# Optimization experiments

Hardware: AMD Instinct MI355X
Metric: run time of the kernel (lower is better)

Reference implementation:

```python
import jax, jax.numpy as jnp
import numpy as np

EPS = 1e-08
PARTIAL_NORM = 1.5
TOPK = 8
SELF_MOD_STEPS = 2


def _layernorm(x, g, b, eps=1e-05):
    mu = jnp.mean(x, axis=-1, keepdims=True)
    var = jnp.mean((x - mu) ** 2, axis=-1, keepdims=True)
    return (x - mu) / jnp.sqrt(var + eps) * g + b


def _spectral_normalize(w, iters=10):
    # mimic torch spectral_norm: divide by top singular value (power iteration)
    u = jnp.ones((w.shape[0],), w.dtype) / np.sqrt(w.shape[0])
    def step(u, _):
        v = w.T @ u
        v = v / (jnp.linalg.norm(v) + 1e-12)
        u2 = w @ v
        u2 = u2 / (jnp.linalg.norm(u2) + 1e-12)
        return u2, None
    u, _ = jax.lax.scan(step, u, None, length=iters)
    v = w.T @ u
    v = v / (jnp.linalg.norm(v) + 1e-12)
    sigma = u @ (w @ v)
    return w / sigma


def setup_inputs() -> dict:
    B, D, H, S, C = 8192, 2048, 1024, 3, 1000
    P = 1024  # proj_dim = ((max(H, D//2)+7)//8)*8
    key = jax.random.key(0)
    ks = jax.random.split(key, 16)
    x = jax.random.normal(ks[0], (B, D), jnp.float32)
    proj_w = jax.random.normal(ks[1], (P, D), jnp.float32) / np.sqrt(D)
    proj_b = jnp.zeros((P,), jnp.float32)
    ln_p_g = jnp.ones((P,), jnp.float32)
    ln_p_b = jnp.zeros((P,), jnp.float32)
    wf_w = jax.random.normal(ks[2], (S, 2 * H, P), jnp.float32) / np.sqrt(P)
    wf_w = jax.vmap(_spectral_normalize)(wf_w)
    wf_b = jax.random.normal(ks[3], (S, 2 * H), jnp.float32) * 0.02
    ln_g = jnp.ones((S, 2 * H), jnp.float32)
    ln_b = jnp.zeros((S, 2 * H), jnp.float32)
    temperature = jnp.ones((1,), jnp.float32)
    phases = jax.random.normal(ks[4], (S, 1), jnp.float32) * 0.5
    gate_w = jax.random.normal(ks[5], (H, H), jnp.float32) / np.sqrt(H)
    gate_b = jnp.zeros((H,), jnp.float32)
    cls_w1 = jax.random.normal(ks[6], (H, H), jnp.float32) / np.sqrt(H)
    cls_b1 = jnp.zeros((H,), jnp.float32)
    cls_w2 = jax.random.normal(ks[7], (C, H), jnp.float32) / np.sqrt(H)
    cls_b2 = jnp.zeros((C,), jnp.float32).at[1].set(0.75)
    return {"x": x, "proj_w": proj_w, "proj_b": proj_b, "ln_p_g": ln_p_g,
            "ln_p_b": ln_p_b, "wf_w": wf_w, "wf_b": wf_b, "ln_g": ln_g,
            "ln_b": ln_b, "temperature": temperature, "phases": phases,
            "gate_w": gate_w, "gate_b": gate_b, "cls_w1": cls_w1,
            "cls_b1": cls_b1, "cls_w2": cls_w2, "cls_b2": cls_b2}


def reference(x, proj_w, proj_b, ln_p_g, ln_p_b, wf_w, wf_b, ln_g, ln_b,
              temperature, phases, gate_w, gate_b, cls_w1, cls_b1, cls_w2, cls_b2):
    H = wf_w.shape[1] // 2
    # input projection (dropout is identity at eval)
    h = jax.nn.gelu(_layernorm(x @ proj_w.T + proj_b, ln_p_g, ln_p_b), approximate=False)
    # all wavefunctions at once: [B, S, 2H]
    out = jnp.einsum('bp,sep->bse', h, wf_w) + wf_b[None]
    out = _layernorm(out, ln_g[None], ln_b[None])
    out = jnp.exp(-out * out)  # ArcBell
    alpha, beta = out[..., :H], out[..., H:]
    norm_sq = jnp.sum(alpha ** 2 + beta ** 2, axis=-1, keepdims=True) + EPS
    factor = jnp.sqrt(PARTIAL_NORM ** 2 / norm_sq)
    alpha = alpha * factor
    beta = beta * factor
    phase = phases[None]  # [1, S, 1]
    c, s = jnp.cos(phase), jnp.sin(phase)
    wave_r = alpha * c - beta * s  # [B, S, H]
    wave_i = alpha * s + beta * c
    # cosine-similarity interference weights
    mean_real = jnp.mean(wave_r, axis=1)  # [B, H]
    mean_norm = jnp.sqrt(jnp.sum(mean_real ** 2, axis=-1, keepdims=True)) + EPS  # [B,1]
    wave_norms = jnp.sqrt(jnp.sum(wave_r ** 2, axis=-1, keepdims=True)) + EPS  # [B,S,1]
    dot = jnp.sum(wave_r * mean_real[:, None], axis=-1, keepdims=True)  # [B,S,1]
    cos_sim = (dot / (wave_norms * mean_norm[:, None]))[..., 0]  # [B,S]
    w = jax.nn.softmax(cos_sim / temperature, axis=1)[..., None]  # [B,S,1]
    sup_r = jnp.sum(wave_r * w, axis=1)  # [B,H]
    sup_i = jnp.sum(wave_i * w, axis=1)
    # self-modulation with leaky residual
    for _ in range(SELF_MOD_STEPS):
        mag = jnp.sqrt(sup_r ** 2 + sup_i ** 2 + EPS)
        gate = jax.nn.sigmoid(mag @ gate_w.T + gate_b)
        sup_r = sup_r * gate + sup_r * 0.1
        sup_i = sup_i * gate + sup_i * 0.1
    mag_sq = sup_r ** 2 + sup_i ** 2
    # top-k mask + scatter + renormalize
    _, inds = jax.lax.top_k(mag_sq, TOPK)
    rows = jnp.arange(mag_sq.shape[0])[:, None]
    mask = jnp.zeros_like(mag_sq).at[rows, inds].set(1.0)
    masked = mag_sq * mask
    probs = masked / (jnp.sum(masked, axis=-1, keepdims=True) + EPS)
    # classifier (dropout identity at eval)
    hid = jax.nn.gelu(probs @ cls_w1.T + cls_b1, approximate=False)
    logits = hid @ cls_w2.T + cls_b2
    return logits
```

## Files before the change

kernel.cpp:

```cpp
#include <hip/hip_runtime.h>
#include <cstdint>

typedef __attribute__((ext_vector_type(8))) __bf16 bf16x8;
typedef __attribute__((ext_vector_type(4))) __bf16 bf16x4;
typedef __attribute__((ext_vector_type(4))) float f32x4;
typedef unsigned long long u64;

__device__ __forceinline__ void gld_lds16(const void* g, void* l) {
  __builtin_amdgcn_global_load_lds(
      (const __attribute__((address_space(1))) void*)g,
      (__attribute__((address_space(3))) void*)l, 16, 0, 0);
}

__device__ __forceinline__ float block_sum(float v, float* scr) {
#pragma unroll
  for (int off = 32; off > 0; off >>= 1) v += __shfl_down(v, off, 64);
  const int w = threadIdx.x >> 6;
  __syncthreads();
  if ((threadIdx.x & 63) == 0) scr[w] = v;
  __syncthreads();
  float s = 0.f;
  const int nw = blockDim.x >> 6;
  for (int i = 0; i < nw; ++i) s += scr[i];
  return s;
}

template <int N>
__device__ __forceinline__ void block_sumN(float* v, float* scr) {
#pragma unroll
  for (int i = 0; i < N; ++i)
#pragma unroll
    for (int m = 1; m < 64; m <<= 1) v[i] += __shfl_xor(v[i], m, 64);
  const int w = threadIdx.x >> 6;
  __syncthreads();
  if ((threadIdx.x & 63) == 0)
#pragma unroll
    for (int i = 0; i < N; ++i) scr[w * N + i] = v[i];
  __syncthreads();
#pragma unroll
  for (int i = 0; i < N; ++i) {
    float s = 0.f;
    for (int ww = 0; ww < 4; ++ww) s += scr[ww * N + i];
    v[i] = s;
  }
}

__device__ __forceinline__ float gelu_fast(float x) {
  const float ax = fabsf(x) * 0.70710678118654752f;
  const float t = 1.f / (1.f + 0.3275911f * ax);
  const float e = __expf(-ax * ax);
  float poly = 1.061405429f;
  poly = poly * t - 1.453152027f;
  poly = poly * t + 1.421413741f;
  poly = poly * t - 0.284496736f;
  poly = poly * t + 0.254829592f;
  const float erfax = 1.f - poly * t * e;
  const float er = copysignf(erfax, x);
  return 0.5f * x * (1.f + er);
}

__global__ __launch_bounds__(256) void k_cast_bf16(const float* __restrict__ in,
                                                   __bf16* __restrict__ out) {
  const long i = ((long)blockIdx.x * 256 + threadIdx.x) * 4;
  f32x4 v = *(const f32x4*)(in + i);
  bf16x4 o = {(__bf16)v[0], (__bf16)v[1], (__bf16)v[2], (__bf16)v[3]};
  *(bf16x4*)(out + i) = o;
}

__global__ __launch_bounds__(256) void k_cast_weights(
    const float* __restrict__ pw, __bf16* __restrict__ w1b,
    const float* __restrict__ wfw, __bf16* __restrict__ wfwb,
    const float* __restrict__ gw, __bf16* __restrict__ gwb) {
  const int bid = blockIdx.x;
  const float* in;
  __bf16* out;
  long base;
  if (bid < 2048) { in = pw; out = w1b; base = (long)bid * 1024; }
  else if (bid < 8192) { in = wfw; out = wfwb; base = (long)(bid - 2048) * 1024; }
  else { in = gw; out = gwb; base = (long)(bid - 8192) * 1024; }
  const long i = base + threadIdx.x * 4;
  f32x4 v = *(const f32x4*)(in + i);
  bf16x4 o = {(__bf16)v[0], (__bf16)v[1], (__bf16)v[2], (__bf16)v[3]};
  *(bf16x4*)(out + i) = o;
}

__global__ __launch_bounds__(256) void k_cast_pad(const float* __restrict__ in,
                                                  __bf16* __restrict__ out,
                                                  int rows_real, int cols) {
  const long i = ((long)blockIdx.x * 256 + threadIdx.x) * 4;
  const int row = (int)(i / cols);
  const int col = (int)(i % cols);
  bf16x4 o;
  if (row < rows_real) {
    f32x4 v = *(const f32x4*)(in + (long)row * cols + col);
    o = (bf16x4){(__bf16)v[0], (__bf16)v[1], (__bf16)v[2], (__bf16)v[3]};
  } else {
    o = (bf16x4){(__bf16)0.f, (__bf16)0.f, (__bf16)0.f, (__bf16)0.f};
  }
  *(bf16x4*)(out + i) = o;
}

__global__ __launch_bounds__(256) void k_transpose1k(const float* __restrict__ in,
                                                     float* __restrict__ out) {
  __shared__ float t[32][33];
  const int tx = threadIdx.x & 31;
  const int ty = threadIdx.x >> 5;
  const int r0 = blockIdx.y * 32, c0 = blockIdx.x * 32;
#pragma unroll
  for (int k = 0; k < 4; ++k)
    t[ty + 8 * k][tx] = in[(long)(r0 + ty + 8 * k) * 1024 + c0 + tx];
  __syncthreads();
#pragma unroll
  for (int k = 0; k < 4; ++k)
    out[(long)(c0 + ty + 8 * k) * 1024 + r0 + tx] = t[tx][ty + 8 * k];
}

__global__ __launch_bounds__(512, 1) void k_gemm256_bt(
    const __bf16* __restrict__ A, const __bf16* __restrict__ B,
    const float* __restrict__ bias, __bf16* __restrict__ C,
    int M, int N, int K) {
  __shared__ __align__(16) __bf16 lds[2][2][256 * 64];
  const int tid = threadIdx.x;
  const int lane = tid & 63;
  const int wid = tid >> 6;
  const int wr = wid >> 2;
  const int wc = wid & 3;
  const int gx = gridDim.x, gy = gridDim.y;
  const int lin = blockIdx.y * gx + blockIdx.x;
  const int xcd = lin & 7;
  const int local = lin >> 3;
  const int byq = gy >> 3;
  const int bx = local / byq;
  const int by = xcd * byq + (local % byq);
  const int m0 = by * 256, n0 = bx * 256;
  const int fr = lane & 15;
  const int fx = lane >> 4;
  const int px = lane & 7;

  const __bf16* Abase = A + (long)m0 * K;
  const __bf16* Bbase = B + (long)n0 * K;

  auto stage_q = [&](int slot, int kt, int mat, int half) {
    const __bf16* src = (mat ? Bbase : Abase) + kt * 64;
#pragma unroll
    for (int q = 0; q < 2; ++q) {
      const int idx = q * 512 + tid;
      const int r = idx >> 3;
      const int pblk = idx & 7;
      const int row = half * 128 + r;
      const int lblk = pblk ^ (r & 7);
      gld_lds16(src + (long)row * K + lblk * 8,
                (char*)&lds[slot][mat][row * 64 + pblk * 8]);
    }
  };
  auto frag = [&](int slot, int mat, int row, int ks) -> bf16x8 {
    return *(const bf16x8*)&lds[slot][mat][row * 64 + ((((ks << 2) + fx) ^ px) << 3)];
  };

  f32x4 acc[8][4] = {};
  const int nt = K >> 6;
#pragma unroll
  for (int qp = 0; qp < 4; ++qp) stage_q(0, 0, qp >> 1, qp & 1);

  const int arow = wr * 128 + fr;
  const int brow = wc * 64 + fr;

  for (int t = 0; t < nt; ++t) {
    const int sc = t & 1, sn = sc ^ 1;
    if (t + 1 < nt) {
#pragma unroll
      for (int qp = 0; qp < 4; ++qp) stage_q(sn, t + 1, qp >> 1, qp & 1);
      asm volatile("s_waitcnt vmcnt(8)" ::: "memory");
    } else {
      asm volatile("s_waitcnt vmcnt(0)" ::: "memory");
    }
    __builtin_amdgcn_sched_barrier(0);
    __builtin_amdgcn_s_barrier();
    bf16x8 b0[4], b1[4];
#pragma unroll
    for (int j = 0; j < 4; ++j) {
      b0[j] = frag(sc, 1, brow + j * 16, 0);
      b1[j] = frag(sc, 1, brow + j * 16, 1);
    }
    __builtin_amdgcn_s_setprio(1);
#pragma unroll
    for (int im = 0; im < 8; ++im) {
      bf16x8 x0 = frag(sc, 0, arow + im * 16, 0);
      bf16x8 x1 = frag(sc, 0, arow + im * 16, 1);
#pragma unroll
      for (int j = 0; j < 4; ++j) {
        acc[im][j] = __builtin_amdgcn_mfma_f32_16x16x32_bf16(x0, b0[j], acc[im][j], 0, 0, 0);
        acc[im][j] = __builtin_amdgcn_mfma_f32_16x16x32_bf16(x1, b1[j], acc[im][j], 0, 0, 0);
      }
    }
    __builtin_amdgcn_s_setprio(0);
    __builtin_amdgcn_s_barrier();
  }

  __bf16* cb = (__bf16*)&lds[0][0][0];
  const int lm0 = wr * 128 + fx * 4;
  const int lc0 = wc * 64 + fr;
#pragma unroll
  for (int j = 0; j < 4; ++j) {
    const float bv = bias[n0 + lc0 + j * 16];
#pragma unroll
    for (int im = 0; im < 8; ++im)
#pragma unroll
      for (int r = 0; r < 4; ++r)
        cb[(lm0 + im * 16 + r) * 256 + lc0 + j * 16] = (__bf16)(acc[im][j][r] + bv);
  }
  __syncthreads();
#pragma unroll
  for (int q = 0; q < 16; ++q) {
    const int idx = q * 512 + tid;
    const int row = idx >> 5;
    const int c8 = (idx & 31) * 8;
    *(f32x4*)(C + (long)(m0 + row) * N + n0 + c8) = *(const f32x4*)(cb + row * 256 + c8);
  }
}

template <int EPI, int BM>
__global__ __launch_bounds__(256) void k_gemm_bt(
    const __bf16* __restrict__ A, const __bf16* __restrict__ B,
    const float* __restrict__ bias, void* __restrict__ Cout,
    int M, int N, int K, int Nreal,
    float* __restrict__ msq, __bf16* __restrict__ magOut) {
  constexpr int MR = BM / 32;
  constexpr int STAGE_B = (2 * BM * 32 + 2 * 128 * 32) * 2;
  constexpr int CB_B = BM * 64 * 4;
  constexpr int SMEM_B = STAGE_B > CB_B ? STAGE_B : CB_B;
  __shared__ __align__(16) char smem[SMEM_B];
  __bf16* As = (__bf16*)smem;
  __bf16* Bs = (__bf16*)(smem + (size_t)2 * BM * 32 * 2);
  float* cb = (float*)smem;
  const int tid = threadIdx.x;
  const int lane = tid & 63;
  const int wid = tid >> 6;
  const int wr = wid >> 1, wc = wid & 1;

  const int gx = gridDim.x, gy = gridDim.y;
  const int nwg = gx * gy;
  int bx, by;
  if ((nwg & 7) == 0) {
    const int lin = blockIdx.y * gx + blockIdx.x;
    const int cpx = nwg >> 3;
    const int w = (lin & 7) * cpx + (lin >> 3);
    bx = w / gy;
    by = w % gy;
  } else {
    bx = blockIdx.x;
    by = blockIdx.y;
  }
  const int m0 = by * BM;
  const int n0 = bx * 128;
  const int frow = lane & 15;
  const int fk = (lane >> 4) * 8;
  f32x4 acc[MR][4] = {};

  auto stage = [&](int buf, int k0) {
    const __bf16* Ab = A + (long)m0 * K + k0;
    const __bf16* Bb = B + (long)n0 * K + k0;
    __bf16* Asb = As + buf * BM * 32;
    __bf16* Bsb = Bs + buf * 128 * 32;
#pragma unroll
    for (int q = 0; q < BM / 64; ++q) {
      const int idx = q * 256 + tid;
      const int row = idx >> 2;
      const int col = (idx & 3) * 8;
      gld_lds16(Ab + (long)row * K + col, (char*)Asb + idx * 16);
    }
#pragma unroll
    for (int q = 0; q < 2; ++q) {
      const int idx = q * 256 + tid;
      const int row = idx >> 2;
      const int col = (idx & 3) * 8;
      gld_lds16(Bb + (long)row * K + col, (char*)Bsb + idx * 16);
    }
  };

  const int nt = K >> 5;
  int cur = 0;
  stage(0, 0);
  __syncthreads();
  for (int t = 0; t < nt; ++t) {
    if (t + 1 < nt) stage(cur ^ 1, (t + 1) << 5);
    bf16x8 af[MR], bfr[4];
#pragma unroll
    for (int i = 0; i < MR; ++i)
      af[i] = *(const bf16x8*)(As + cur * BM * 32 + (wr * (BM / 2) + i * 16 + frow) * 32 + fk);
#pragma unroll
    for (int i = 0; i < 4; ++i)
      bfr[i] = *(const bf16x8*)(Bs + cur * 128 * 32 + (wc * 64 + i * 16 + frow) * 32 + fk);
#pragma unroll
    for (int im = 0; im < MR; ++im)
#pragma unroll
      for (int in = 0; in < 4; ++in)
        acc[im][in] = __builtin_amdgcn_mfma_f32_16x16x32_bf16(af[im], bfr[in],
                                                              acc[im][in], 0, 0, 0);
    __syncthreads();
    cur ^= 1;
  }

  if (EPI == 0 || EPI == 6 || EPI == 7) {
#pragma unroll 1
    for (int h = 0; h < 2; ++h) {
      __syncthreads();
      if (wc == h) {
#pragma unroll
        for (int in = 0; in < 4; ++in) {
          const int col = n0 + h * 64 + in * 16 + frow;
          const float bv = (col < Nreal) ? bias[col] : 0.f;
          const int lcc = in * 16 + frow;
#pragma unroll
          for (int im = 0; im < MR; ++im)
#pragma unroll
            for (int r = 0; r < 4; ++r) {
              const float v = acc[im][in][r] + bv;
              float sv;
              if (EPI == 0) {
                sv = v;
              } else {
                const float f = 1.f / (1.f + __expf(-v)) + 0.1f;
                sv = f * f;
              }
              cb[(wr * (BM / 2) + (lane >> 4) * 4 + im * 16 + r) * 64 + lcc] = sv;
            }
        }
      }
      __syncthreads();
#pragma unroll
      for (int q = 0; q < BM / 16; ++q) {
        const int idx = q * 256 + tid;
        const int row = idx >> 4;
        const int c4 = (idx & 15) * 4;
        const int gc = n0 + h * 64 + c4;
        if (EPI == 0) {
          if (gc < Nreal)
            *(f32x4*)((float*)Cout + (long)(m0 + row) * Nreal + gc) =
                *(const f32x4*)(cb + row * 64 + c4);
        } else {
          const long gix = (long)(m0 + row) * Nreal + gc;
          f32x4 m = *(const f32x4*)(msq + gix);
          const f32x4 f2 = *(const f32x4*)(cb + row * 64 + c4);
          m[0] *= f2[0]; m[1] *= f2[1]; m[2] *= f2[2]; m[3] *= f2[3];
          *(f32x4*)(msq + gix) = m;
          if (EPI == 6) {
            bf16x4 mg = {(__bf16)sqrtf(m[0] + 1e-8f), (__bf16)sqrtf(m[1] + 1e-8f),
                         (__bf16)sqrtf(m[2] + 1e-8f), (__bf16)sqrtf(m[3] + 1e-8f)};
            *(bf16x4*)(magOut + gix) = mg;
          }
        }
      }
    }
  } else {
    const int crow0 = m0 + wr * (BM / 2) + (lane >> 4) * 4;
    const int ccol0 = n0 + wc * 64 + (lane & 15);
#pragma unroll
    for (int in = 0; in < 4; ++in) {
      const int col = ccol0 + in * 16;
      if (col >= Nreal) continue;
      const float bv = bias[col];
#pragma unroll
      for (int im = 0; im < MR; ++im) {
#pragma unroll
        for (int r = 0; r < 4; ++r) {
          const long row = crow0 + im * 16 + r;
          ((__bf16*)Cout)[row * Nreal + col] = (__bf16)(acc[im][in][r] + bv);
        }
      }
    }
  }
}

__global__ __launch_bounds__(256) void k_ln_gelu(const float* __restrict__ y,
                                                 const float* __restrict__ g,
                                                 const float* __restrict__ b,
                                                 __bf16* __restrict__ h) {
  __shared__ float scr[8];
  const int tid = threadIdx.x;
  const long row = blockIdx.x;
  const float* yr = y + row * 1024;
  f32x4 v = *(const f32x4*)(yr + tid * 4);
  float ls = v[0] + v[1] + v[2] + v[3];
  const float mu = block_sum(ls, scr) * (1.f / 1024.f);
  float lss = 0.f;
#pragma unroll
  for (int j = 0; j < 4; ++j) {
    const float d = v[j] - mu;
    lss += d * d;
  }
  const float var = block_sum(lss, scr) * (1.f / 1024.f);
  const float rstd = rsqrtf(var + 1e-5f);
  bf16x4 o;
#pragma unroll
  for (int j = 0; j < 4; ++j) {
    const int c = tid * 4 + j;
    const float t = (v[j] - mu) * rstd * g[c] + b[c];
    o[j] = (__bf16)gelu_fast(t);
  }
  *(bf16x4*)(h + row * 1024 + tid * 4) = o;
}

__global__ __launch_bounds__(256) void k_stage_c(
    const __bf16* __restrict__ outb, const float* __restrict__ ln_g,
    const float* __restrict__ ln_b, const float* __restrict__ phases,
    const float* __restrict__ temp, float* __restrict__ msq,
    __bf16* __restrict__ mag0, int b0) {
  __shared__ float scr[28];
  const int t = threadIdx.x;
  const long b = blockIdx.x;

  float xa[3][4], xb[3][4];
  float red[6];
#pragma unroll
  for (int s = 0; s < 3; ++s) {
    const __bf16* src = outb + b * 6144 + s * 2048;
    const bf16x4 va = *(const bf16x4*)(src + t * 4);
    const bf16x4 vb = *(const bf16x4*)(src + 1024 + t * 4);
    float sum = 0.f, ssq = 0.f;
#pragma unroll
    for (int j = 0; j < 4; ++j) {
      xa[s][j] = (float)va[j];
      xb[s][j] = (float)vb[j];
      sum += xa[s][j] + xb[s][j];
      ssq += xa[s][j] * xa[s][j] + xb[s][j] * xb[s][j];
    }
    red[2 * s] = sum;
    red[2 * s + 1] = ssq;
  }
  block_sumN<6>(red, scr);

  float ag[3][4], bg[3][4];
  float nsq[3];
#pragma unroll
  for (int s = 0; s < 3; ++s) {
    const float mu = red[2 * s] * (1.f / 2048.f);
    const float var = red[2 * s + 1] * (1.f / 2048.f) - mu * mu;
    const float rstd = rsqrtf(var + 1e-5f);
    const f32x4 ga = *(const f32x4*)(ln_g + s * 2048 + t * 4);
    const f32x4 ba = *(const f32x4*)(ln_b + s * 2048 + t * 4);
    const f32x4 gb = *(const f32x4*)(ln_g + s * 2048 + 1024 + t * 4);
    const f32x4 bb = *(const f32x4*)(ln_b + s * 2048 + 1024 + t * 4);
    float acc = 0.f;
#pragma unroll
    for (int j = 0; j < 4; ++j) {
      const float ya = (xa[s][j] - mu) * rstd * ga[j] + ba[j];
      const float yb = (xb[s][j] - mu) * rstd * gb[j] + bb[j];
      ag[s][j] = __expf(-ya * ya);
      bg[s][j] = __expf(-yb * yb);
      acc += ag[s][j] * ag[s][j] + bg[s][j] * bg[s][j];
    }
    nsq[s] = acc;
  }
  block_sumN<3>(nsq, scr);

  float wr[3][4], wi[3][4];
#pragma unroll
  for (int s = 0; s < 3; ++s) {
    const float factor = sqrtf(2.25f / (nsq[s] + 1e-8f));
    const float ph = phases[s];
    const float cs = __cosf(ph), sn = __sinf(ph);
#pragma unroll
    for (int j = 0; j < 4; ++j) {
      const float a = ag[s][j] * factor;
      const float b2 = bg[s][j] * factor;
      wr[s][j] = a * cs - b2 * sn;
      wi[s][j] = a * sn + b2 * cs;
    }
  }

  float mr[4];
  float dw[7] = {0.f, 0.f, 0.f, 0.f, 0.f, 0.f, 0.f};
#pragma unroll
  for (int j = 0; j < 4; ++j) {
    const float m = (wr[0][j] + wr[1][j] + wr[2][j]) * (1.f / 3.f);
    mr[j] = m;
    dw[6] += m * m;
    dw[0] += wr[0][j] * mr[j]; dw[1] += wr[0][j] * wr[0][j];
    dw[2] += wr[1][j] * mr[j]; dw[3] += wr[1][j] * wr[1][j];
    dw[4] += wr[2][j] * mr[j]; dw[5] += wr[2][j] * wr[2][j];
  }
  block_sumN<7>(dw, scr);
  const float mnorm = sqrtf(dw[6]) + 1e-8f;
  const float T = temp[0];
  const float c0 = dw[0] / ((sqrtf(dw[1]) + 1e-8f) * mnorm) / T;
  const float c1 = dw[2] / ((sqrtf(dw[3]) + 1e-8f) * mnorm) / T;
  const float c2 = dw[4] / ((sqrtf(dw[5]) + 1e-8f) * mnorm) / T;
  const float mx = fmaxf(c0, fmaxf(c1, c2));
  const float e0 = __expf(c0 - mx), e1 = __expf(c1 - mx), e2 = __expf(c2 - mx);
  const float inv = 1.f / (e0 + e1 + e2);
  const float w0 = e0 * inv, w1 = e1 * inv, w2 = e2 * inv;

  const long base = (long)(b0 + b) * 1024 + t * 4;
  f32x4 m2o;
  bf16x4 mgo;
#pragma unroll
  for (int j = 0; j < 4; ++j) {
    const float sr = wr[0][j] * w0 + wr[1][j] * w1 + wr[2][j] * w2;
    const float si = wi[0][j] * w0 + wi[1][j] * w1 + wi[2][j] * w2;
    const float m2 = sr * sr + si * si;
    m2o[j] = m2;
    mgo[j] = (__bf16)sqrtf(m2 + 1e-8f);
  }
  *(f32x4*)(msq + base) = m2o;
  *(bf16x4*)(mag0 + base) = mgo;
}

__global__ __launch_bounds__(256) void k_topk_cls1(
    const float* __restrict__ msq,
    const float* __restrict__ w1t, const float* __restrict__ b1,
    __bf16* __restrict__ hid) {
  __shared__ u64 candk[32];
  __shared__ u64 selk_s[8];
  __shared__ float ssum_s;
  const int tid = threadIdx.x;
  const int lane = tid & 63;
  const int wv = tid >> 6;
  const long b = blockIdx.x;

  f32x4 mv = *(const f32x4*)(msq + b * 1024 + tid * 4);
  u64 key[4];
#pragma unroll
  for (int j = 0; j < 4; ++j)
    key[j] = ((u64)__float_as_uint(mv[j]) << 32) | (unsigned)(~(unsigned)(tid * 4 + j));
  u64 lm = key[0];
  int jm = 0;
#pragma unroll
  for (int j = 1; j < 4; ++j)
    if (key[j] > lm) { lm = key[j]; jm = j; }

#pragma unroll 1
  for (int it = 0; it < 8; ++it) {
    u64 bk = lm;
#pragma unroll
    for (int m = 1; m < 64; m <<= 1) {
      const u64 ok = __shfl_xor(bk, m, 64);
      bk = ok > bk ? ok : bk;
    }
    if (lane == 0) candk[wv * 8 + it] = bk;
    if (bk == lm) {
      key[jm] = 0ULL;
      lm = key[0]; jm = 0;
#pragma unroll
      for (int j = 1; j < 4; ++j)
        if (key[j] > lm) { lm = key[j]; jm = j; }
    }
  }
  __syncthreads();

  if (wv == 0) {
    u64 ck = (lane < 32) ? candk[lane] : 0ULL;
    float ss = 0.f;
#pragma unroll 1
    for (int it = 0; it < 8; ++it) {
      u64 bk = ck;
#pragma unroll
      for (int m = 1; m < 64; m <<= 1) {
        const u64 ok = __shfl_xor(bk, m, 64);
        bk = ok > bk ? ok : bk;
      }
      if (ck == bk) ck = 0ULL;
      if (lane == 0) {
        selk_s[it] = bk;
        ss += __uint_as_float((unsigned)(bk >> 32));
      }
    }
    if (lane == 0) ssum_s = ss;
  }
  __syncthreads();

  const float denom = 1.f / (ssum_s + 1e-8f);
  float p[8];
  int idx[8];
#pragma unroll
  for (int k = 0; k < 8; ++k) {
    const u64 kk = selk_s[k];
    p[k] = __uint_as_float((unsigned)(kk >> 32)) * denom;
    idx[k] = (int)(~(unsigned)kk & 1023u);
  }

  const int o0 = tid * 4;
  float acc0 = b1[o0], acc1 = b1[o0 + 1], acc2 = b1[o0 + 2], acc3 = b1[o0 + 3];
#pragma unroll
  for (int k = 0; k < 8; ++k) {
    const f32x4 wrow = *(const f32x4*)(w1t + (long)idx[k] * 1024 + o0);
    acc0 += p[k] * wrow[0];
    acc1 += p[k] * wrow[1];
    acc2 += p[k] * wrow[2];
    acc3 += p[k] * wrow[3];
  }
  bf16x4 o = {(__bf16)gelu_fast(acc0), (__bf16)gelu_fast(acc1),
              (__bf16)gelu_fast(acc2), (__bf16)gelu_fast(acc3)};
  *(bf16x4*)(hid + b * 1024 + o0) = o;
}

extern "C" void kernel_launch(void* const* d_in, const int* in_sizes, int n_in,
                              void* d_out, int out_size, void* d_ws, size_t ws_size,
                              hipStream_t stream) {
  const float* x      = (const float*)d_in[0];
  const float* proj_w = (const float*)d_in[1];
  const float* proj_b = (const float*)d_in[2];
  const float* ln_p_g = (const float*)d_in[3];
  const float* ln_p_b = (const float*)d_in[4];
  const float* wf_w   = (const float*)d_in[5];
  const float* wf_b   = (const float*)d_in[6];
  const float* ln_g   = (const float*)d_in[7];
  const float* ln_b   = (const float*)d_in[8];
  const float* temperature = (const float*)d_in[9];
  const float* phases = (const float*)d_in[10];
  const float* gate_w = (const float*)d_in[11];
  const float* gate_b = (const float*)d_in[12];
  const float* cls_w1 = (const float*)d_in[13];
  const float* cls_b1 = (const float*)d_in[14];
  const float* cls_w2 = (const float*)d_in[15];
  const float* cls_b2 = (const float*)d_in[16];
  float* out = (float*)d_out;
  (void)in_sizes; (void)n_in; (void)out_size;

  char* ws = (char*)d_ws;
  const size_t MB = 1024 * 1024;

  if (ws_size >= 196 * MB) {
    __bf16* xb   = (__bf16*)(ws + 0);
    float*  msq  = (float*)(ws + 0);
    float*  y1   = (float*)(ws + 32 * MB);
    __bf16* mag0 = (__bf16*)(ws + 32 * MB);
    __bf16* mag1 = (__bf16*)(ws + 48 * MB);
    __bf16* outb = (__bf16*)(ws + 64 * MB);
    __bf16* hid  = (__bf16*)(ws + 64 * MB);
    float*  w1t  = (float*)(ws + 96 * MB);
    __bf16* hb   = (__bf16*)(ws + 160 * MB);
    __bf16* wfwb = (__bf16*)(ws + 176 * MB);
    __bf16* gwb  = (__bf16*)(ws + 188 * MB);
    __bf16* c2b  = (__bf16*)(ws + 190 * MB);
    __bf16* w1b  = (__bf16*)(ws + 192 * MB);

    k_cast_bf16<<<16384, 256, 0, stream>>>(x, xb);
    k_cast_weights<<<9216, 256, 0, stream>>>(proj_w, w1b, wf_w, wfwb, gate_w, gwb);
    k_cast_pad<<<1024, 256, 0, stream>>>(cls_w2, c2b, 1000, 1024);

    k_gemm_bt<0, 64><<<dim3(8, 128), 256, 0, stream>>>(xb, w1b, proj_b, y1, 8192, 1024, 2048, 1024, nullptr, nullptr);
    k_ln_gelu<<<8192, 256, 0, stream>>>(y1, ln_p_g, ln_p_b, hb);

    k_gemm256_bt<<<dim3(24, 32), 512, 0, stream>>>(hb, wfwb, wf_b, outb, 8192, 6144, 1024);
    k_stage_c<<<8192, 256, 0, stream>>>(outb, ln_g, ln_b, phases, temperature, msq, mag0, 0);

    k_transpose1k<<<dim3(32, 32), 256, 0, stream>>>(cls_w1, w1t);
    k_gemm_bt<6, 64><<<dim3(8, 128), 256, 0, stream>>>(mag0, gwb, gate_b, nullptr, 8192, 1024, 1024, 1024, msq, mag1);
    k_gemm_bt<7, 64><<<dim3(8, 128), 256, 0, stream>>>(mag1, gwb, gate_b, nullptr, 8192, 1024, 1024, 1024, msq, nullptr);

    k_topk_cls1<<<8192, 256, 0, stream>>>(msq, w1t, cls_b1, hid);
    k_gemm_bt<0, 64><<<dim3(8, 128), 256, 0, stream>>>(hid, c2b, cls_b2, out, 8192, 1024, 1024, 1000, nullptr, nullptr);
  } else {
    __bf16* xb   = (__bf16*)(ws + 0);
    float*  msq  = (float*)(ws + 0);
    float*  y1   = (float*)(ws + 32 * MB);
    __bf16* outc = (__bf16*)(ws + 32 * MB);
    __bf16* mag1 = (__bf16*)(ws + 32 * MB);
    __bf16* hid  = (__bf16*)(ws + 48 * MB);
    __bf16* w1b  = (__bf16*)(ws + 64 * MB);
    __bf16* mag0 = (__bf16*)(ws + 64 * MB);
    __bf16* wfwb = (__bf16*)(ws + 96 * MB);
    __bf16* hb   = (__bf16*)(ws + 108 * MB);
    float*  w1t  = (float*)(ws + 108 * MB);
    __bf16* gwb  = (__bf16*)(ws + 124 * MB);
    __bf16* c2b  = (__bf16*)(ws + 126 * MB);

    k_cast_bf16<<<16384, 256, 0, stream>>>(x, xb);
    k_cast_weights<<<9216, 256, 0, stream>>>(proj_w, w1b, wf_w, wfwb, gate_w, gwb);
    k_cast_pad<<<1024, 256, 0, stream>>>(cls_w2, c2b, 1000, 1024);

    k_gemm_bt<0, 64><<<dim3(8, 128), 256, 0, stream>>>(xb, w1b, proj_b, y1, 8192, 1024, 2048, 1024, nullptr, nullptr);
    k_ln_gelu<<<8192, 256, 0, stream>>>(y1, ln_p_g, ln_p_b, hb);

    for (int c = 0; c < 4; ++c) {
      k_gemm_bt<1, 128><<<dim3(48, 16), 256, 0, stream>>>(hb + (size_t)c * 2048 * 1024, wfwb, wf_b,
                                                          outc, 2048, 6144, 1024, 6144, nullptr, nullptr);
      k_stage_c<<<2048, 256, 0, stream>>>(outc, ln_g, ln_b, phases, temperature,
                                          msq, mag0, c * 2048);
    }

    k_transpose1k<<<dim3(32, 32), 256, 0, stream>>>(cls_w1, w1t);
    k_gemm_bt<6, 64><<<dim3(8, 128), 256, 0, stream>>>(mag0, gwb, gate_b, nullptr, 8192, 1024, 1024, 1024, msq, mag1);
    k_gemm_bt<7, 64><<<dim3(8, 128), 256, 0, stream>>>(mag1, gwb, gate_b, nullptr, 8192, 1024, 1024, 1024, msq, nullptr);

    k_topk_cls1<<<8192, 256, 0, stream>>>(msq, w1t, cls_b1, hid);
    k_gemm_bt<0, 64><<<dim3(8, 128), 256, 0, stream>>>(hid, c2b, cls_b2, out, 8192, 1024, 1024, 1000, nullptr, nullptr);
  }
}
```

Baseline: 452.3 us.

## Split GEMM main loop into four quadrant phases interleaving loads with MFMA

Restructures the bf16 GEMM main loop into a four-phase, ping-pong-like schedule. Each phase issues one quarter of the next tile's global-to-LDS loads, reads a subset of A/B fragments, and runs a quadrant of MFMAs. The aim is to overlap global loads and LDS reads with matrix compute instead of staging everything up front per tile. Half of tile t+2 is prefetched into the current slot while it is still being read, which relies on careful barrier placement and adds more barriers per iteration.

```diff
diff --git a/kernel.cpp b/kernel.cpp
--- a/kernel.cpp
+++ b/kernel.cpp
@@ -159,41 +159,105 @@
 
   f32x4 acc[8][4] = {};
   const int nt = K >> 6;
-#pragma unroll
-  for (int qp = 0; qp < 4; ++qp) stage_q(0, 0, qp >> 1, qp & 1);
+  stage_q(0, 0, 0, 0);
+  stage_q(0, 0, 0, 1);
+  stage_q(0, 0, 1, 0);
+  stage_q(0, 0, 1, 1);
+  if (nt > 1) {
+    stage_q(1, 1, 1, 0);
+    stage_q(1, 1, 1, 1);
+    asm volatile("s_waitcnt vmcnt(4)" ::: "memory");
+  } else {
+    asm volatile("s_waitcnt vmcnt(0)" ::: "memory");
+  }
+  __builtin_amdgcn_sched_barrier(0);
+  __builtin_amdgcn_s_barrier();
 
   const int arow = wr * 128 + fr;
   const int brow = wc * 64 + fr;
+  bf16x8 af[4][2], bl[2][2], bh[2][2];
 
   for (int t = 0; t < nt; ++t) {
-    const int sc = t & 1, sn = sc ^ 1;
-    if (t + 1 < nt) {
-#pragma unroll
-      for (int qp = 0; qp < 4; ++qp) stage_q(sn, t + 1, qp >> 1, qp & 1);
-      asm volatile("s_waitcnt vmcnt(8)" ::: "memory");
+    const int s = t & 1;
+    if (t + 1 < nt) stage_q(s ^ 1, t + 1, 0, 0);
+#pragma unroll
+    for (int i = 0; i < 4; ++i) {
+      af[i][0] = frag(s, 0, arow + i * 16, 0);
+      af[i][1] = frag(s, 0, arow + i * 16, 1);
+    }
+#pragma unroll
+    for (int j = 0; j < 2; ++j) {
+      bl[j][0] = frag(s, 1, brow + j * 16, 0);
+      bl[j][1] = frag(s, 1, brow + j * 16, 1);
+    }
+    __builtin_amdgcn_s_barrier();
+    asm volatile("s_waitcnt lgkmcnt(0)" ::: "memory");
+    __builtin_amdgcn_sched_barrier(0);
+    __builtin_amdgcn_s_setprio(1);
+#pragma unroll
+    for (int i = 0; i < 4; ++i)
+#pragma unroll
+      for (int j = 0; j < 2; ++j) {
+        acc[i][j] = __builtin_amdgcn_mfma_f32_16x16x32_bf16(af[i][0], bl[j][0], acc[i][j], 0, 0, 0);
+        acc[i][j] = __builtin_amdgcn_mfma_f32_16x16x32_bf16(af[i][1], bl[j][1], acc[i][j], 0, 0, 0);
+      }
+    __builtin_amdgcn_s_setprio(0);
+    __builtin_amdgcn_s_barrier();
+    if (t + 1 < nt) stage_q(s ^ 1, t + 1, 0, 1);
+#pragma unroll
+    for (int j = 0; j < 2; ++j) {
+      bh[j][0] = frag(s, 1, brow + (j + 2) * 16, 0);
+      bh[j][1] = frag(s, 1, brow + (j + 2) * 16, 1);
+    }
+    __builtin_amdgcn_s_barrier();
+    asm volatile("s_waitcnt lgkmcnt(0)" ::: "memory");
+    __builtin_amdgcn_sched_barrier(0);
+    __builtin_amdgcn_s_setprio(1);
+#pragma unroll
+    for (int i = 0; i < 4; ++i)
+#pragma unroll
+      for (int j = 0; j < 2; ++j) {
+        acc[i][j + 2] = __builtin_amdgcn_mfma_f32_16x16x32_bf16(af[i][0], bh[j][0], acc[i][j + 2], 0, 0, 0);
+        acc[i][j + 2] = __builtin_amdgcn_mfma_f32_16x16x32_bf16(af[i][1], bh[j][1], acc[i][j + 2], 0, 0, 0);
+      }
+    __builtin_amdgcn_s_setprio(0);
+    __builtin_amdgcn_s_barrier();
+    if (t + 2 < nt) stage_q(s, t + 2, 1, 0);
+#pragma unroll
+    for (int i = 0; i < 4; ++i) {
+      af[i][0] = frag(s, 0, arow + (i + 4) * 16, 0);
+      af[i][1] = frag(s, 0, arow + (i + 4) * 16, 1);
+    }
+    __builtin_amdgcn_s_barrier();
+    asm volatile("s_waitcnt lgkmcnt(0)" ::: "memory");
+    __builtin_amdgcn_sched_barrier(0);
+    __builtin_amdgcn_s_setprio(1);
+#pragma unroll
+    for (int i = 0; i < 4; ++i)
+#pragma unroll
+      for (int j = 0; j < 2; ++j) {
+        acc[i + 4][j + 2] = __builtin_amdgcn_mfma_f32_16x16x32_bf16(af[i][0], bh[j][0], acc[i + 4][j + 2], 0, 0, 0);
+        acc[i + 4][j + 2] = __builtin_amdgcn_mfma_f32_16x16x32_bf16(af[i][1], bh[j][1], acc[i + 4][j + 2], 0, 0, 0);
+      }
+    __builtin_amdgcn_s_setprio(0);
+    __builtin_amdgcn_s_barrier();
+    if (t + 2 < nt) stage_q(s, t + 2, 1, 1);
+    __builtin_amdgcn_s_barrier();
+    __builtin_amdgcn_s_setprio(1);
+#pragma unroll
+    for (int i = 0; i < 4; ++i)
+#pragma unroll
+      for (int j = 0; j < 2; ++j) {
+        acc[i + 4][j] = __builtin_amdgcn_mfma_f32_16x16x32_bf16(af[i][0], bl[j][0], acc[i + 4][j], 0, 0, 0);
+        acc[i + 4][j] = __builtin_amdgcn_mfma_f32_16x16x32_bf16(af[i][1], bl[j][1], acc[i + 4][j], 0, 0, 0);
+      }
+    __builtin_amdgcn_s_setprio(0);
+    if (t + 2 < nt) {
+      asm volatile("s_waitcnt vmcnt(4)" ::: "memory");
     } else {
       asm volatile("s_waitcnt vmcnt(0)" ::: "memory");
     }
     __builtin_amdgcn_sched_barrier(0);
-    __builtin_amdgcn_s_barrier();
-    bf16x8 b0[4], b1[4];
-#pragma unroll
-    for (int j = 0; j < 4; ++j) {
-      b0[j] = frag(sc, 1, brow + j * 16, 0);
-      b1[j] = frag(sc, 1, brow + j * 16, 1);
-    }
-    __builtin_amdgcn_s_setprio(1);
-#pragma unroll
-    for (int im = 0; im < 8; ++im) {
-      bf16x8 x0 = frag(sc, 0, arow + im * 16, 0);
-      bf16x8 x1 = frag(sc, 0, arow + im * 16, 1);
-#pragma unroll
-      for (int j = 0; j < 4; ++j) {
-        acc[im][j] = __builtin_amdgcn_mfma_f32_16x16x32_bf16(x0, b0[j], acc[im][j], 0, 0, 0);
-        acc[im][j] = __builtin_amdgcn_mfma_f32_16x16x32_bf16(x1, b1[j], acc[im][j], 0, 0, 0);
-      }
-    }
-    __builtin_amdgcn_s_setprio(0);
     __builtin_amdgcn_s_barrier();
   }
 
```

Measured after the change: 451.4 us. About the same (-0.2%).
